# Optimization experiments

Hardware: AMD Instinct MI355X
Metric: run time of the kernel (lower is better)

The kernel has to match this reference:

```python
import jax, jax.numpy as jnp
import numpy as np

NUM_ANCHORS = 3
NUM_CLASSES = 80
STRIDES = (16.0, 32.0)
ANCHORS = (
    jnp.array([[12.64, 19.39], [37.88, 51.48], [55.71, 138.31]], dtype=jnp.float32),
    jnp.array([[126.91, 78.23], [131.57, 214.55], [279.92, 258.87]], dtype=jnp.float32),
)


def conv1x1(x, w, b):
    # x: [B,C,H,W], w: [O,C], b: [O] -> [B,O,H,W]
    return jnp.einsum('bchw,oc->bohw', x, w) + b[None, :, None, None]


def decode_level(reg, obj, cls, stride, anchors):
    # reg: [B,12,H,W], obj: [B,3,H,W], cls: [B,80,H,W]
    B, _, H, W = reg.shape
    r = reg.transpose(0, 2, 3, 1).reshape(B, H, W, NUM_ANCHORS, 4)
    o = obj.transpose(0, 2, 3, 1).reshape(B, H, W, NUM_ANCHORS, 1)
    c = cls.transpose(0, 2, 3, 1)[:, :, :, None, :]  # [B,H,W,1,80], shared across anchors
    gy, gx = jnp.meshgrid(jnp.arange(H, dtype=reg.dtype), jnp.arange(W, dtype=reg.dtype), indexing='ij')
    grid = jnp.stack([gx, gy], axis=-1)[None, :, :, None, :]  # [1,H,W,1,2] = (x, y)
    xy = (jax.nn.sigmoid(r[..., :2]) * 2.0 - 0.5 + grid) * stride
    wh = (jax.nn.sigmoid(r[..., 2:4]) * 2.0) ** 2 * anchors  # anchors [3,2] broadcast
    ob = jax.nn.sigmoid(o)
    cp = jnp.broadcast_to(jax.nn.softmax(c, axis=-1), (B, H, W, NUM_ANCHORS, NUM_CLASSES))
    boxes = jnp.concatenate([xy, wh, ob, cp], axis=-1)  # [B,H,W,3,85]
    return boxes.reshape(B, H * W * NUM_ANCHORS, 5 + NUM_CLASSES)


def setup_inputs() -> dict:
    key = jax.random.key(0)
    ks = jax.random.split(key, 12)
    B, C = 64, 72
    inp = {
        'feat_reg0': jax.random.normal(ks[0], (B, C, 40, 40), jnp.float32),
        'feat_obj0': jax.random.normal(ks[1], (B, C, 40, 40), jnp.float32),
        'feat_cls0': jax.random.normal(ks[2], (B, C, 40, 40), jnp.float32),
        'feat_reg1': jax.random.normal(ks[3], (B, C, 20, 20), jnp.float32),
        'feat_obj1': jax.random.normal(ks[4], (B, C, 20, 20), jnp.float32),
        'feat_cls1': jax.random.normal(ks[5], (B, C, 20, 20), jnp.float32),
        'w_reg': jax.random.normal(ks[6], (4 * NUM_ANCHORS, C), jnp.float32) * 0.05,
        'b_reg': jax.random.normal(ks[7], (4 * NUM_ANCHORS,), jnp.float32) * 0.05,
        'w_obj': jax.random.normal(ks[8], (NUM_ANCHORS, C), jnp.float32) * 0.05,
        'b_obj': jax.random.normal(ks[9], (NUM_ANCHORS,), jnp.float32) * 0.05,
        'w_cls': jax.random.normal(ks[10], (NUM_CLASSES, C), jnp.float32) * 0.05,
        'b_cls': jax.random.normal(ks[11], (NUM_CLASSES,), jnp.float32) * 0.05,
    }
    return inp


def reference(feat_reg0, feat_obj0, feat_cls0, feat_reg1, feat_obj1, feat_cls1,
              w_reg, b_reg, w_obj, b_obj, w_cls, b_cls):
    feats = ((feat_reg0, feat_obj0, feat_cls0), (feat_reg1, feat_obj1, feat_cls1))
    outs = []
    for i, (fr, fo, fc) in enumerate(feats):
        reg = conv1x1(fr, w_reg, b_reg)
        obj = conv1x1(fo, w_obj, b_obj)
        cls = conv1x1(fc, w_cls, b_cls)
        outs.append(decode_level(reg, obj, cls, STRIDES[i], ANCHORS[i]))
    return jnp.concatenate(outs, axis=1)  # [B, 6000, 85]
```

## Files before the change

kernel.cpp:

```cpp
#include <hip/hip_runtime.h>
#include <math.h>

#define C_IN 72
#define RST 97
#define NFRAG 21
#define STG_T (16 * C_IN)
#define SMEM_BYTES 6912

typedef short short8  __attribute__((ext_vector_type(8)));
typedef float floatx4 __attribute__((ext_vector_type(4)));

#define GLD4(dst, ptr) \
    asm volatile("global_load_dwordx4 %0, %1, off" : "=v"(dst) : "v"(ptr))

__device__ __forceinline__ unsigned short f2bf(float f) {
    unsigned u = __float_as_uint(f);
    u += 0x7FFFu + ((u >> 16) & 1u);
    return (unsigned short)(u >> 16);
}
__device__ __forceinline__ float sigf(float x) {
    return __builtin_amdgcn_rcpf(1.0f + __expf(-x));
}

__global__ void __launch_bounds__(256)
build_bfrags_kernel(const float* __restrict__ w_reg,
                    const float* __restrict__ w_obj,
                    const float* __restrict__ w_cls,
                    short8* __restrict__ frags)
{
    int idx = blockIdx.x * 256 + threadIdx.x;
    if (idx >= NFRAG * 64) return;
    int lane = idx & 63;
    int fi   = idx >> 6;
    int tile = fi / 3, kc = fi - tile * 3;
    int m = lane & 15, quad = lane >> 4;
    const float* wrow;
    bool valid = true;
    if (tile == 0)      { wrow = w_reg + m * C_IN; valid = (m < 12); }
    else if (tile == 1) { wrow = w_obj + m * C_IN; valid = (m < 3); }
    else                { wrow = w_cls + ((tile - 2) * 16 + m) * C_IN; }
    short8 r = {0, 0, 0, 0, 0, 0, 0, 0};
    if (valid && !(kc == 2 && quad != 0)) {
        const float* p = wrow + kc * 32 + quad * 8;
#pragma unroll
        for (int j = 0; j < 8; ++j) r[j] = (short)f2bf(p[j]);
    }
    frags[fi * 64 + lane] = r;
}

__global__ void __launch_bounds__(64, 3)
yolo_head_kernel(const float* __restrict__ fr0, const float* __restrict__ fo0, const float* __restrict__ fc0,
                 const float* __restrict__ fr1, const float* __restrict__ fo1, const float* __restrict__ fc1,
                 const float* __restrict__ b_reg, const float* __restrict__ b_obj,
                 const float* __restrict__ b_cls,
                 const short8* __restrict__ wfrag,
                 float* __restrict__ out)
{
    __shared__ __align__(16) unsigned char smem[SMEM_BYTES];
    unsigned short* const stage = (unsigned short*)smem;
    float* const row = (float*)smem;

    const int pid  = blockIdx.x;
    const int bid  = (pid & 7) * 1000 + (pid >> 3);
    const int lane = threadIdx.x;
    const int m    = lane & 15;
    const int quad = lane >> 4;
    const int chg  = lane >> 2;
    const int pg   = lane & 3;

    int lvl, b, pos0, HW, W, LO;
    const float *fr, *fo, *fc;
    if (bid < 6400) {
        lvl = 0; b = bid / 100; pos0 = (bid - b * 100) * 16;
        HW = 1600; W = 40; LO = 0; fr = fr0; fo = fo0; fc = fc0;
    } else {
        int t = bid - 6400;
        lvl = 1; b = t / 25; pos0 = (t - b * 25) * 16;
        HW = 400; W = 20; LO = 4800; fr = fr1; fo = fo1; fc = fc1;
    }
    const float STRIDE = lvl ? 32.0f : 16.0f;

    const int fbase = b * C_IN * HW + pos0 + pg * 4;
    const float* srcs[3] = {fr, fo, fc};
    floatx4 ld[3][5];
#pragma unroll
    for (int t = 0; t < 3; ++t) {
        const float* sp = srcs[t] + fbase;
#pragma unroll
        for (int g = 0; g < 4; ++g) {
            const float* p = sp + (g * 16 + chg) * HW;
            GLD4(ld[t][g], p);
        }
    }
    if (lane < 32) {
#pragma unroll
        for (int t = 0; t < 3; ++t) {
            const float* p = srcs[t] + fbase + (64 + chg) * HW;
            GLD4(ld[t][4], p);
        }
    }
    asm volatile("s_waitcnt vmcnt(0)" ::: "memory");
    __builtin_amdgcn_sched_barrier(0);

#pragma unroll
    for (int t = 0; t < 3; ++t) {
#pragma unroll
        for (int g = 0; g < 4; ++g)
#pragma unroll
            for (int i = 0; i < 4; ++i)
                stage[t * STG_T + (pg * 4 + i) * C_IN + g * 16 + chg] = f2bf(ld[t][g][i]);
        if (lane < 32)
#pragma unroll
            for (int i = 0; i < 4; ++i)
                stage[t * STG_T + (pg * 4 + i) * C_IN + 64 + chg] = f2bf(ld[t][4][i]);
    }

    short8 wf[NFRAG];
#pragma unroll
    for (int fi = 0; fi < NFRAG; ++fi) {
        const short8* p = wfrag + fi * 64 + lane;
        GLD4(wf[fi], p);
    }
    const float brg = b_reg[m < 12 ? m : 0];
    const float bob = b_obj[m < 3 ? m : 0];
    float bcl[5];
#pragma unroll
    for (int nt = 0; nt < 5; ++nt) bcl[nt] = b_cls[nt * 16 + m];

    __asm__ volatile("s_waitcnt lgkmcnt(0)" ::: "memory");

    short8 af[3][3];
#pragma unroll
    for (int t = 0; t < 3; ++t) {
        const unsigned short* tp = stage + t * STG_T + m * C_IN;
        af[t][0] = *(const short8*)(tp + quad * 8);
        af[t][1] = *(const short8*)(tp + 32 + quad * 8);
        short8 v = *(const short8*)(tp + 64);
        if (quad) v = (short8){0, 0, 0, 0, 0, 0, 0, 0};
        af[t][2] = v;
    }
    __asm__ volatile("s_waitcnt lgkmcnt(0)" ::: "memory");

    asm volatile("s_waitcnt vmcnt(0)" ::: "memory");
    __builtin_amdgcn_sched_barrier(0);

    floatx4 accR = {0, 0, 0, 0}, accO = {0, 0, 0, 0}, accC[5];
#pragma unroll
    for (int kc = 0; kc < 3; ++kc)
        accR = __builtin_amdgcn_mfma_f32_16x16x32_bf16(af[0][kc], wf[0 * 3 + kc], accR, 0, 0, 0);
#pragma unroll
    for (int kc = 0; kc < 3; ++kc)
        accO = __builtin_amdgcn_mfma_f32_16x16x32_bf16(af[1][kc], wf[1 * 3 + kc], accO, 0, 0, 0);
#pragma unroll
    for (int nt = 0; nt < 5; ++nt) {
        floatx4 a4 = {0, 0, 0, 0};
#pragma unroll
        for (int kc = 0; kc < 3; ++kc)
            a4 = __builtin_amdgcn_mfma_f32_16x16x32_bf16(af[2][kc], wf[(nt + 2) * 3 + kc], a4, 0, 0, 0);
        accC[nt] = a4;
    }

    const int a_ = m >> 2, k_ = m & 3;
    float anch;
    {
        float e0, e1;
        if (lvl == 0) { e0 = a_ == 0 ? 12.64f  : a_ == 1 ? 37.88f  : 55.71f;
                        e1 = a_ == 0 ? 19.39f  : a_ == 1 ? 51.48f  : 138.31f; }
        else          { e0 = a_ == 0 ? 126.91f : a_ == 1 ? 131.57f : 279.92f;
                        e1 = a_ == 0 ? 78.23f  : a_ == 1 ? 214.55f : 258.87f; }
        anch = (k_ == 3) ? e1 : e0;
    }

#pragma unroll
    for (int i = 0; i < 4; ++i) {
        const int prel = quad * 4 + i;
        const int pg_  = pos0 + prel;
        const int gyi  = lvl ? (pg_ / 20) : (pg_ / 40);
        const float gx = (float)(pg_ - gyi * W);
        const float gy = (float)gyi;

        if (m < 12) {
            float sg = sigf(accR[i] + brg);
            float v;
            if (k_ == 0)      v = (sg * 2.0f - 0.5f + gx) * STRIDE;
            else if (k_ == 1) v = (sg * 2.0f - 0.5f + gy) * STRIDE;
            else { float t2 = sg * 2.0f; v = t2 * t2 * anch; }
            row[prel * RST + a_ * 5 + k_] = v;
        }
        if (m < 3)
            row[prel * RST + m * 5 + 4] = sigf(accO[i] + bob);

        float e[5];
        float s = 0.f;
#pragma unroll
        for (int nt = 0; nt < 5; ++nt) {
            e[nt] = __expf(accC[nt][i] + bcl[nt]);
            s += e[nt];
        }
        s += __shfl_xor(s, 1, 16);
        s += __shfl_xor(s, 2, 16);
        s += __shfl_xor(s, 4, 16);
        s += __shfl_xor(s, 8, 16);
        const float inv = __builtin_amdgcn_rcpf(s);
#pragma unroll
        for (int nt = 0; nt < 5; ++nt)
            row[prel * RST + 15 + nt * 16 + m] = e[nt] * inv;
    }
    __asm__ volatile("s_waitcnt lgkmcnt(0)" ::: "memory");

    int wi0[4];
#pragma unroll
    for (int j = 0; j < 4; ++j) {
        int f = lane + 64 * j;
        int k = (f > 254) ? 0 : f;
        int a  = (k >= 85) + (k >= 170);
        int kk = k - a * 85;
        wi0[j] = (kk < 5) ? (a * 5 + kk) : (15 + (kk - 5));
    }
    float* outp = out + ((size_t)b * 510000 + LO * 85 + pos0 * 255);
    for (int p = 0; p < 16; ++p) {
        const float* rr = row + p * RST;
        float* po = outp + p * 255 + lane;
#pragma unroll
        for (int j = 0; j < 4; ++j) {
            if (!(lane == 63 && j == 3))
                po[64 * j] = rr[wi0[j]];
        }
    }
}

extern "C" void kernel_launch(void* const* d_in, const int* in_sizes, int n_in,
                              void* d_out, int out_size, void* d_ws, size_t ws_size,
                              hipStream_t stream) {
    (void)in_sizes; (void)n_in; (void)ws_size; (void)out_size;
    const float* fr0  = (const float*)d_in[0];
    const float* fo0  = (const float*)d_in[1];
    const float* fc0  = (const float*)d_in[2];
    const float* fr1  = (const float*)d_in[3];
    const float* fo1  = (const float*)d_in[4];
    const float* fc1  = (const float*)d_in[5];
    const float* wreg = (const float*)d_in[6];
    const float* breg = (const float*)d_in[7];
    const float* wobj = (const float*)d_in[8];
    const float* bobj = (const float*)d_in[9];
    const float* wcls = (const float*)d_in[10];
    const float* bcls = (const float*)d_in[11];
    float* out = (float*)d_out;
    short8* frags = (short8*)d_ws;

    build_bfrags_kernel<<<6, 256, 0, stream>>>(wreg, wobj, wcls, frags);

    yolo_head_kernel<<<8000, 64, 0, stream>>>(
        fr0, fo0, fc0, fr1, fo1, fc1,
        breg, bobj, bcls, frags, out);
}
```

Baseline: 249.1 us.

## Make waves persistent over four tiles with prefetch, LDS weights, and vector stores

The grid becomes 500 blocks of four waves, and each wave now handles four consecutive 16-position tiles instead of one. The next tile's feature loads are issued before the MFMA and epilogue of the current tile, so global latency overlaps with compute. Weight fragments are staged once per block in LDS instead of being loaded into registers per wave. The output write becomes a contiguous 16-byte vector store with computed index remapping. The tradeoffs are more registers held for prefetch, a larger LDS footprint, and fewer blocks to hide latency.

```diff
diff --git a/kernel.cpp b/kernel.cpp
--- a/kernel.cpp
+++ b/kernel.cpp
@@ -5,7 +5,8 @@
 #define RST 97
 #define NFRAG 21
 #define STG_T (16 * C_IN)
-#define SMEM_BYTES 6912
+#define WF_BYTES (NFRAG * 64 * 16)
+#define WAVE_LDS 6912
 
 typedef short short8  __attribute__((ext_vector_type(8)));
 typedef float floatx4 __attribute__((ext_vector_type(4)));
@@ -48,7 +49,7 @@
     frags[fi * 64 + lane] = r;
 }
 
-__global__ void __launch_bounds__(64, 3)
+__global__ void __launch_bounds__(256)
 yolo_head_kernel(const float* __restrict__ fr0, const float* __restrict__ fo0, const float* __restrict__ fc0,
                  const float* __restrict__ fr1, const float* __restrict__ fo1, const float* __restrict__ fc1,
                  const float* __restrict__ b_reg, const float* __restrict__ b_obj,
@@ -56,109 +57,31 @@
                  const short8* __restrict__ wfrag,
                  float* __restrict__ out)
 {
-    __shared__ __align__(16) unsigned char smem[SMEM_BYTES];
-    unsigned short* const stage = (unsigned short*)smem;
-    float* const row = (float*)smem;
-
-    const int pid  = blockIdx.x;
-    const int bid  = (pid & 7) * 1000 + (pid >> 3);
-    const int lane = threadIdx.x;
+    __shared__ __align__(16) unsigned char smem[WF_BYTES + 4 * WAVE_LDS];
+    short8* const wfl = (short8*)smem;
+    const int tid  = threadIdx.x;
+    const int wid  = tid >> 6;
+    const int lane = tid & 63;
+    unsigned short* const stage = (unsigned short*)(smem + WF_BYTES + wid * WAVE_LDS);
+    float*          const row   = (float*)         (smem + WF_BYTES + wid * WAVE_LDS);
+
+    for (int j = tid; j < NFRAG * 64; j += 256) wfl[j] = wfrag[j];
+    __syncthreads();
+
     const int m    = lane & 15;
     const int quad = lane >> 4;
     const int chg  = lane >> 2;
     const int pg   = lane & 3;
 
-    int lvl, b, pos0, HW, W, LO;
+    const int wg = blockIdx.x * 4 + wid;
+    int lvl, HW, W, LO, sbase;
     const float *fr, *fo, *fc;
-    if (bid < 6400) {
-        lvl = 0; b = bid / 100; pos0 = (bid - b * 100) * 16;
-        HW = 1600; W = 40; LO = 0; fr = fr0; fo = fo0; fc = fc0;
-    } else {
-        int t = bid - 6400;
-        lvl = 1; b = t / 25; pos0 = (t - b * 25) * 16;
-        HW = 400; W = 20; LO = 4800; fr = fr1; fo = fo1; fc = fc1;
-    }
+    if (wg < 1600) { lvl = 0; HW = 1600; W = 40; LO = 0;    sbase = wg * 4;
+                     fr = fr0; fo = fo0; fc = fc0; }
+    else           { lvl = 1; HW = 400;  W = 20; LO = 4800; sbase = (wg - 1600) * 4;
+                     fr = fr1; fo = fo1; fc = fc1; }
     const float STRIDE = lvl ? 32.0f : 16.0f;
-
-    const int fbase = b * C_IN * HW + pos0 + pg * 4;
     const float* srcs[3] = {fr, fo, fc};
-    floatx4 ld[3][5];
-#pragma unroll
-    for (int t = 0; t < 3; ++t) {
-        const float* sp = srcs[t] + fbase;
-#pragma unroll
-        for (int g = 0; g < 4; ++g) {
-            const float* p = sp + (g * 16 + chg) * HW;
-            GLD4(ld[t][g], p);
-        }
-    }
-    if (lane < 32) {
-#pragma unroll
-        for (int t = 0; t < 3; ++t) {
-            const float* p = srcs[t] + fbase + (64 + chg) * HW;
-            GLD4(ld[t][4], p);
-        }
-    }
-    asm volatile("s_waitcnt vmcnt(0)" ::: "memory");
-    __builtin_amdgcn_sched_barrier(0);
-
-#pragma unroll
-    for (int t = 0; t < 3; ++t) {
-#pragma unroll
-        for (int g = 0; g < 4; ++g)
-#pragma unroll
-            for (int i = 0; i < 4; ++i)
-                stage[t * STG_T + (pg * 4 + i) * C_IN + g * 16 + chg] = f2bf(ld[t][g][i]);
-        if (lane < 32)
-#pragma unroll
-            for (int i = 0; i < 4; ++i)
-                stage[t * STG_T + (pg * 4 + i) * C_IN + 64 + chg] = f2bf(ld[t][4][i]);
-    }
-
-    short8 wf[NFRAG];
-#pragma unroll
-    for (int fi = 0; fi < NFRAG; ++fi) {
-        const short8* p = wfrag + fi * 64 + lane;
-        GLD4(wf[fi], p);
-    }
-    const float brg = b_reg[m < 12 ? m : 0];
-    const float bob = b_obj[m < 3 ? m : 0];
-    float bcl[5];
-#pragma unroll
-    for (int nt = 0; nt < 5; ++nt) bcl[nt] = b_cls[nt * 16 + m];
-
-    __asm__ volatile("s_waitcnt lgkmcnt(0)" ::: "memory");
-
-    short8 af[3][3];
-#pragma unroll
-    for (int t = 0; t < 3; ++t) {
-        const unsigned short* tp = stage + t * STG_T + m * C_IN;
-        af[t][0] = *(const short8*)(tp + quad * 8);
-        af[t][1] = *(const short8*)(tp + 32 + quad * 8);
-        short8 v = *(const short8*)(tp + 64);
-        if (quad) v = (short8){0, 0, 0, 0, 0, 0, 0, 0};
-        af[t][2] = v;
-    }
-    __asm__ volatile("s_waitcnt lgkmcnt(0)" ::: "memory");
-
-    asm volatile("s_waitcnt vmcnt(0)" ::: "memory");
-    __builtin_amdgcn_sched_barrier(0);
-
-    floatx4 accR = {0, 0, 0, 0}, accO = {0, 0, 0, 0}, accC[5];
-#pragma unroll
-    for (int kc = 0; kc < 3; ++kc)
-        accR = __builtin_amdgcn_mfma_f32_16x16x32_bf16(af[0][kc], wf[0 * 3 + kc], accR, 0, 0, 0);
-#pragma unroll
-    for (int kc = 0; kc < 3; ++kc)
-        accO = __builtin_amdgcn_mfma_f32_16x16x32_bf16(af[1][kc], wf[1 * 3 + kc], accO, 0, 0, 0);
-#pragma unroll
-    for (int nt = 0; nt < 5; ++nt) {
-        floatx4 a4 = {0, 0, 0, 0};
-#pragma unroll
-        for (int kc = 0; kc < 3; ++kc)
-            a4 = __builtin_amdgcn_mfma_f32_16x16x32_bf16(af[2][kc], wf[(nt + 2) * 3 + kc], a4, 0, 0, 0);
-        accC[nt] = a4;
-    }
 
     const int a_ = m >> 2, k_ = m & 3;
     float anch;
@@ -170,61 +93,147 @@
                         e1 = a_ == 0 ? 78.23f  : a_ == 1 ? 214.55f : 258.87f; }
         anch = (k_ == 3) ? e1 : e0;
     }
+    const float brg = b_reg[m < 12 ? m : 0];
+    const float bob = b_obj[m < 3 ? m : 0];
+    float bcl[5];
+#pragma unroll
+    for (int nt = 0; nt < 5; ++nt) bcl[nt] = b_cls[nt * 16 + m];
+
+    floatx4 ld[3][5];
+    auto issueT1 = [&](int S) {
+        int b, pos0;
+        if (lvl == 0) { b = S / 100; pos0 = (S - b * 100) * 16; }
+        else          { b = S / 25;  pos0 = (S - b * 25) * 16; }
+        const int fb = b * C_IN * HW + pos0 + pg * 4;
+#pragma unroll
+        for (int t = 0; t < 3; ++t) {
+            const float* sp = srcs[t] + fb;
+#pragma unroll
+            for (int g = 0; g < 4; ++g) {
+                const float* p = sp + (g * 16 + chg) * HW;
+                GLD4(ld[t][g], p);
+            }
+        }
+        if (lane < 32) {
+#pragma unroll
+            for (int t = 0; t < 3; ++t) {
+                const float* p = srcs[t] + fb + (64 + chg) * HW;
+                GLD4(ld[t][4], p);
+            }
+        }
+    };
+
+    issueT1(sbase);
 
 #pragma unroll
     for (int i = 0; i < 4; ++i) {
-        const int prel = quad * 4 + i;
-        const int pg_  = pos0 + prel;
-        const int gyi  = lvl ? (pg_ / 20) : (pg_ / 40);
-        const float gx = (float)(pg_ - gyi * W);
-        const float gy = (float)gyi;
-
-        if (m < 12) {
-            float sg = sigf(accR[i] + brg);
-            float v;
-            if (k_ == 0)      v = (sg * 2.0f - 0.5f + gx) * STRIDE;
-            else if (k_ == 1) v = (sg * 2.0f - 0.5f + gy) * STRIDE;
-            else { float t2 = sg * 2.0f; v = t2 * t2 * anch; }
-            row[prel * RST + a_ * 5 + k_] = v;
-        }
-        if (m < 3)
-            row[prel * RST + m * 5 + 4] = sigf(accO[i] + bob);
-
-        float e[5];
-        float s = 0.f;
+        const int S = sbase + i;
+        int b, pos0;
+        if (lvl == 0) { b = S / 100; pos0 = (S - b * 100) * 16; }
+        else          { b = S / 25;  pos0 = (S - b * 25) * 16; }
+
+        if (i == 0) asm volatile("s_waitcnt vmcnt(0)" ::: "memory");
+        else        asm volatile("s_waitcnt vmcnt(16)" ::: "memory");
+        __builtin_amdgcn_sched_barrier(0);
+
+#pragma unroll
+        for (int t = 0; t < 3; ++t) {
+#pragma unroll
+            for (int g = 0; g < 4; ++g)
+#pragma unroll
+                for (int ii = 0; ii < 4; ++ii)
+                    stage[t * STG_T + (pg * 4 + ii) * C_IN + g * 16 + chg] = f2bf(ld[t][g][ii]);
+            if (lane < 32)
+#pragma unroll
+                for (int ii = 0; ii < 4; ++ii)
+                    stage[t * STG_T + (pg * 4 + ii) * C_IN + 64 + chg] = f2bf(ld[t][4][ii]);
+        }
+        asm volatile("s_waitcnt lgkmcnt(0)" ::: "memory");
+
+        short8 af[3][3];
+#pragma unroll
+        for (int t = 0; t < 3; ++t) {
+            const unsigned short* tp = stage + t * STG_T + m * C_IN;
+            af[t][0] = *(const short8*)(tp + quad * 8);
+            af[t][1] = *(const short8*)(tp + 32 + quad * 8);
+            short8 v = *(const short8*)(tp + 64);
+            if (quad) v = (short8){0, 0, 0, 0, 0, 0, 0, 0};
+            af[t][2] = v;
+        }
+        asm volatile("s_waitcnt lgkmcnt(0)" ::: "memory");
+
+        if (i < 3) issueT1(S + 1);
+
+        floatx4 accR = {0, 0, 0, 0}, accO = {0, 0, 0, 0}, accC[5];
+#pragma unroll
+        for (int kc = 0; kc < 3; ++kc)
+            accR = __builtin_amdgcn_mfma_f32_16x16x32_bf16(af[0][kc], wfl[(0 * 3 + kc) * 64 + lane], accR, 0, 0, 0);
+#pragma unroll
+        for (int kc = 0; kc < 3; ++kc)
+            accO = __builtin_amdgcn_mfma_f32_16x16x32_bf16(af[1][kc], wfl[(1 * 3 + kc) * 64 + lane], accO, 0, 0, 0);
 #pragma unroll
         for (int nt = 0; nt < 5; ++nt) {
-            e[nt] = __expf(accC[nt][i] + bcl[nt]);
-            s += e[nt];
-        }
-        s += __shfl_xor(s, 1, 16);
-        s += __shfl_xor(s, 2, 16);
-        s += __shfl_xor(s, 4, 16);
-        s += __shfl_xor(s, 8, 16);
-        const float inv = __builtin_amdgcn_rcpf(s);
-#pragma unroll
-        for (int nt = 0; nt < 5; ++nt)
-            row[prel * RST + 15 + nt * 16 + m] = e[nt] * inv;
-    }
-    __asm__ volatile("s_waitcnt lgkmcnt(0)" ::: "memory");
-
-    int wi0[4];
-#pragma unroll
-    for (int j = 0; j < 4; ++j) {
-        int f = lane + 64 * j;
-        int k = (f > 254) ? 0 : f;
-        int a  = (k >= 85) + (k >= 170);
-        int kk = k - a * 85;
-        wi0[j] = (kk < 5) ? (a * 5 + kk) : (15 + (kk - 5));
-    }
-    float* outp = out + ((size_t)b * 510000 + LO * 85 + pos0 * 255);
-    for (int p = 0; p < 16; ++p) {
-        const float* rr = row + p * RST;
-        float* po = outp + p * 255 + lane;
-#pragma unroll
-        for (int j = 0; j < 4; ++j) {
-            if (!(lane == 63 && j == 3))
-                po[64 * j] = rr[wi0[j]];
+            floatx4 a4 = {0, 0, 0, 0};
+#pragma unroll
+            for (int kc = 0; kc < 3; ++kc)
+                a4 = __builtin_amdgcn_mfma_f32_16x16x32_bf16(af[2][kc], wfl[((nt + 2) * 3 + kc) * 64 + lane], a4, 0, 0, 0);
+            accC[nt] = a4;
+        }
+
+#pragma unroll
+        for (int ii = 0; ii < 4; ++ii) {
+            const int prel = quad * 4 + ii;
+            const int pg_  = pos0 + prel;
+            const int gyi  = lvl ? (pg_ / 20) : (pg_ / 40);
+            const float gx = (float)(pg_ - gyi * W);
+            const float gy = (float)gyi;
+
+            if (m < 12) {
+                float sg = sigf(accR[ii] + brg);
+                float v;
+                if (k_ == 0)      v = (sg * 2.0f - 0.5f + gx) * STRIDE;
+                else if (k_ == 1) v = (sg * 2.0f - 0.5f + gy) * STRIDE;
+                else { float t2 = sg * 2.0f; v = t2 * t2 * anch; }
+                row[prel * RST + a_ * 5 + k_] = v;
+            }
+            if (m < 3)
+                row[prel * RST + m * 5 + 4] = sigf(accO[ii] + bob);
+
+            float e[5];
+            float s = 0.f;
+#pragma unroll
+            for (int nt = 0; nt < 5; ++nt) {
+                e[nt] = __expf(accC[nt][ii] + bcl[nt]);
+                s += e[nt];
+            }
+            s += __shfl_xor(s, 1, 16);
+            s += __shfl_xor(s, 2, 16);
+            s += __shfl_xor(s, 4, 16);
+            s += __shfl_xor(s, 8, 16);
+            const float inv = __builtin_amdgcn_rcpf(s);
+#pragma unroll
+            for (int nt = 0; nt < 5; ++nt)
+                row[prel * RST + 15 + nt * 16 + m] = e[nt] * inv;
+        }
+        asm volatile("s_waitcnt lgkmcnt(0)" ::: "memory");
+
+        float* outp = out + ((size_t)b * 510000 + LO * 85 + pos0 * 255);
+#pragma unroll
+        for (int s = 0; s < 16; ++s) {
+            if (!(s == 15 && lane >= 60)) {
+                floatx4 v;
+#pragma unroll
+                for (int j = 0; j < 4; ++j) {
+                    const int F  = s * 256 + lane * 4 + j;
+                    const int p  = (F * 4113) >> 20;
+                    const int k  = F - p * 255;
+                    const int a  = (k >= 85) + (k >= 170);
+                    const int kk = k - a * 85;
+                    const int wi = (kk < 5) ? (a * 5 + kk) : (15 + (kk - 5));
+                    v[j] = row[p * RST + wi];
+                }
+                *(floatx4*)(outp + s * 256 + lane * 4) = v;
+            }
         }
     }
 }
@@ -250,7 +259,7 @@
 
     build_bfrags_kernel<<<6, 256, 0, stream>>>(wreg, wobj, wcls, frags);
 
-    yolo_head_kernel<<<8000, 64, 0, stream>>>(
+    yolo_head_kernel<<<500, 256, 0, stream>>>(
         fr0, fo0, fc0, fr1, fo1, fc1,
         breg, bobj, bcls, frags, out);
 }
```

Result: slower. 257.1 us (+3.2%).
